# Kernel optimization log

Measured on AMD Instinct MI355X. Metric: run time of the kernel, lower is better.

The kernel has to match this reference:

```python
import jax, jax.numpy as jnp
import numpy as np

B, S, D, H = 2, 2048, 1024, 16
DK = D // H
WINDOW = 256


def _make_mask():
    # causal local-window sparsity: attend to j in (i-WINDOW, i]
    i = np.arange(S)[:, None]
    j = np.arange(S)[None, :]
    m = (j <= i) & (i - j < WINDOW)
    return jnp.asarray(m)


def setup_inputs() -> dict:
    key = jax.random.key(0)
    ks = jax.random.split(key, 9)
    sw = 1.0 / np.sqrt(D)
    return {
        "x": jax.random.normal(ks[0], (B, S, D), dtype=jnp.float32),
        "wq": jax.random.normal(ks[1], (D, D), dtype=jnp.float32) * sw,
        "bq": jnp.zeros((D,), dtype=jnp.float32),
        "wk": jax.random.normal(ks[2], (D, D), dtype=jnp.float32) * sw,
        "bk": jnp.zeros((D,), dtype=jnp.float32),
        "wv": jax.random.normal(ks[3], (D, D), dtype=jnp.float32) * sw,
        "bv": jnp.zeros((D,), dtype=jnp.float32),
        "wo": jax.random.normal(ks[4], (D, D), dtype=jnp.float32) * sw,
        "bo": jnp.zeros((D,), dtype=jnp.float32),
        "mask": _make_mask(),
    }


def reference(x, wq, bq, wk, bk, wv, bv, wo, bo, mask):
    b, s, d = x.shape
    # projections (torch Linear: x @ W.T + b), split heads -> [b, h, s, dk]
    def proj(w, bias):
        return (x @ w.T + bias).reshape(b, s, H, DK).transpose(0, 2, 1, 3)

    q = proj(wq, bq)
    k = proj(wk, bk)
    v = proj(wv, bv)

    scores = jnp.einsum("bhqd,bhkd->bhqk", q, k) / jnp.sqrt(jnp.float32(DK))
    scores = jnp.where(mask, scores, -jnp.inf)  # mask broadcasts over b, h
    attn = jax.nn.softmax(scores, axis=-1)
    out = jnp.einsum("bhqk,bhkd->bhqd", attn, v)
    out = out.transpose(0, 2, 1, 3).reshape(b, s, d)
    return out @ wo.T + bo
```

## Files before the change

kernel.cpp:

```cpp
#include <hip/hip_runtime.h>

#define S_LEN 2048
#define DMODEL 1024
#define NHEADS 16
#define WIN 256

typedef unsigned short u16;
typedef unsigned int u32;
typedef __attribute__((ext_vector_type(8))) __bf16 bf16x8;
typedef __attribute__((ext_vector_type(4))) float f32x4;
typedef __attribute__((ext_vector_type(8))) u16 u16x8;
typedef __attribute__((ext_vector_type(4))) u16 u16x4;

__device__ __forceinline__ u16 f2bf(float f) {
  u32 u = __builtin_bit_cast(u32, f);
  u += 0x7fffu + ((u >> 16) & 1u);
  return (u16)(u >> 16);
}

#define GLDS16(g, l) __builtin_amdgcn_global_load_lds( \
    (const __attribute__((address_space(1))) void*)(g), \
    (__attribute__((address_space(3))) void*)(l), 16, 0, 0)

__global__ __launch_bounds__(256) void cast_all(
    const float* __restrict__ x, const float* __restrict__ wq, const float* __restrict__ wk,
    const float* __restrict__ wv, const float* __restrict__ wo,
    u16* __restrict__ xb, u16* __restrict__ wqb, u16* __restrict__ wkb,
    u16* __restrict__ wvb, u16* __restrict__ wob) {
  const int e = (blockIdx.x * 256 + threadIdx.x) * 4;
  const float* src; u16* dst; int off;
  if (e < (1 << 22)) { src = x; dst = xb; off = e; }
  else {
    int r = e - (1 << 22);
    int seg = r >> 20; off = r & ((1 << 20) - 1);
    src = (seg == 0) ? wq : (seg == 1) ? wk : (seg == 2) ? wv : wo;
    dst = (seg == 0) ? wqb : (seg == 1) ? wkb : (seg == 2) ? wvb : wob;
  }
  float4 v = *(const float4*)(src + off);
  u16x4 o = { f2bf(v.x), f2bf(v.y), f2bf(v.z), f2bf(v.w) };
  *(u16x4*)(dst + off) = o;
}

__global__ __launch_bounds__(256) void gemm_nt(
    const u16* __restrict__ A,
    const u16* __restrict__ B0, const u16* __restrict__ B1, const u16* __restrict__ B2,
    const float* __restrict__ bias0, const float* __restrict__ bias1, const float* __restrict__ bias2,
    u16* __restrict__ C0, u16* __restrict__ C1, u16* __restrict__ C2,
    const int M, const int N, const int K)
{
  const u16* Bt; const float* bias; u16* C;
  if (blockIdx.z == 0)      { Bt = B0; bias = bias0; C = C0; }
  else if (blockIdx.z == 1) { Bt = B1; bias = bias1; C = C1; }
  else                      { Bt = B2; bias = bias2; C = C2; }

  __shared__ u16 As[2][128 * 32];
  __shared__ u16 Bs[2][128 * 32];

  const int t = threadIdx.x;
  const int row0 = blockIdx.x * 128;
  const int col0 = blockIdx.y * 128;
  const int lane = t & 63, lo = lane & 15, hi = lane >> 4;
  const int wv = t >> 6;
  const int wr = (wv >> 1) * 64, wc = (wv & 1) * 64;

  f32x4 acc[4][4];
  #pragma unroll
  for (int i = 0; i < 4; ++i)
    #pragma unroll
    for (int j = 0; j < 4; ++j) acc[i][j] = (f32x4)0.0f;

  const int NT = K >> 5;

  auto stage = [&](int buf, int kt) {
    const int kof = kt * 32;
    #pragma unroll
    for (int c = 0; c < 2; ++c) {
      const int off = t * 16 + c * 4096;
      const int r = off >> 6;
      const int ke = (off & 63) >> 1;
      GLDS16(A  + (size_t)(row0 + r) * K + (kof + ke), (u16*)As + buf * (128 * 32) + (off >> 1));
      GLDS16(Bt + (size_t)(col0 + r) * K + (kof + ke), (u16*)Bs + buf * (128 * 32) + (off >> 1));
    }
  };

  stage(0, 0);
  int cur = 0;
  for (int kt = 0; kt < NT; ++kt) {
    __syncthreads();
    if (kt + 1 < NT) stage(cur ^ 1, kt + 1);
    bf16x8 af[4], bfr[4];
    #pragma unroll
    for (int mi = 0; mi < 4; ++mi)
      af[mi] = *(const bf16x8*)&As[cur][(wr + mi * 16 + lo) * 32 + hi * 8];
    #pragma unroll
    for (int ni = 0; ni < 4; ++ni)
      bfr[ni] = *(const bf16x8*)&Bs[cur][(wc + ni * 16 + lo) * 32 + hi * 8];
    #pragma unroll
    for (int mi = 0; mi < 4; ++mi)
      #pragma unroll
      for (int ni = 0; ni < 4; ++ni)
        acc[mi][ni] = __builtin_amdgcn_mfma_f32_16x16x32_bf16(af[mi], bfr[ni], acc[mi][ni], 0, 0, 0);
    cur ^= 1;
  }

  #pragma unroll
  for (int mi = 0; mi < 4; ++mi) {
    #pragma unroll
    for (int ni = 0; ni < 4; ++ni) {
      const int col = col0 + wc + ni * 16 + lo;
      const float bv = bias[col];
      #pragma unroll
      for (int r = 0; r < 4; ++r) {
        const int row = row0 + wr + mi * 16 + hi * 4 + r;
        C[(size_t)row * N + col] = f2bf(acc[mi][ni][r] + bv);
      }
    }
  }
}

__global__ __launch_bounds__(256) void gemm_out64(
    const u16* __restrict__ A, const u16* __restrict__ Bt,
    const float* __restrict__ bias, float* __restrict__ C)
{
  constexpr int N = 1024, K = 1024;

  __shared__ u16 As[2][128 * 32];
  __shared__ u16 Bs[2][64 * 32];

  int id = blockIdx.y * gridDim.x + blockIdx.x;
  int wgid = (id & 7) * 64 + (id >> 3);
  const int row0 = (wgid >> 4) * 128;
  const int col0 = (wgid & 15) * 64;

  const int t = threadIdx.x;
  const int lane = t & 63, lo = lane & 15, hi = lane >> 4;
  const int wv = t >> 6;
  const int wr = (wv >> 1) * 64, wc = (wv & 1) * 32;

  f32x4 acc[4][2];
  #pragma unroll
  for (int i = 0; i < 4; ++i)
    #pragma unroll
    for (int j = 0; j < 2; ++j) acc[i][j] = (f32x4)0.0f;

  auto stage = [&](int buf, int kt) {
    const int kof = kt * 32;
    #pragma unroll
    for (int c = 0; c < 2; ++c) {
      const int off = t * 16 + c * 4096;
      const int r = off >> 6;
      const int ke = (off & 63) >> 1;
      GLDS16(A + (size_t)(row0 + r) * K + (kof + ke), (u16*)As + buf * (128 * 32) + (off >> 1));
    }
    {
      const int off = t * 16;
      const int r = off >> 6;
      const int ke = (off & 63) >> 1;
      GLDS16(Bt + (size_t)(col0 + r) * K + (kof + ke), (u16*)Bs + buf * (64 * 32) + (off >> 1));
    }
  };

  stage(0, 0);
  int cur = 0;
  for (int kt = 0; kt < (K >> 5); ++kt) {
    __syncthreads();
    if (kt + 1 < (K >> 5)) stage(cur ^ 1, kt + 1);
    bf16x8 af[4], bfr[2];
    #pragma unroll
    for (int mi = 0; mi < 4; ++mi)
      af[mi] = *(const bf16x8*)&As[cur][(wr + mi * 16 + lo) * 32 + hi * 8];
    #pragma unroll
    for (int ni = 0; ni < 2; ++ni)
      bfr[ni] = *(const bf16x8*)&Bs[cur][(wc + ni * 16 + lo) * 32 + hi * 8];
    #pragma unroll
    for (int mi = 0; mi < 4; ++mi)
      #pragma unroll
      for (int ni = 0; ni < 2; ++ni)
        acc[mi][ni] = __builtin_amdgcn_mfma_f32_16x16x32_bf16(af[mi], bfr[ni], acc[mi][ni], 0, 0, 0);
    cur ^= 1;
  }

  #pragma unroll
  for (int mi = 0; mi < 4; ++mi) {
    #pragma unroll
    for (int ni = 0; ni < 2; ++ni) {
      const int col = col0 + wc + ni * 16 + lo;
      const float bv = bias[col];
      #pragma unroll
      for (int r = 0; r < 4; ++r) {
        const int row = row0 + wr + mi * 16 + hi * 4 + r;
        C[(size_t)row * N + col] = acc[mi][ni][r] + bv;
      }
    }
  }
}

__device__ __forceinline__ int swzK(int row, int col) {
  int byte = (row << 7) + (col << 1);
  byte ^= (row & 7) << 4;
  return byte >> 1;
}
__device__ __forceinline__ int swzV(int d, int j) {
  int byte = (d << 7) + (j << 1);
  byte ^= ((d & 7) << 4) ^ (((d >> 4) & 3) << 5);
  return byte >> 1;
}

__global__ __launch_bounds__(256) void attn_win(const u16* __restrict__ Q,
                                                const u16* __restrict__ K,
                                                const u16* __restrict__ V,
                                                u16* __restrict__ O) {
  const int qt = blockIdx.x, h = blockIdx.y, b = blockIdx.z;
  const int q0 = qt * 64;
  const int t = threadIdx.x;
  const int wv = t >> 6, lane = t & 63, lo = lane & 15, hi = lane >> 4;

  __shared__ u16 Qs[64 * 64];
  __shared__ u16 Ks[2][64 * 64];
  __shared__ u16 Vt[2][64 * 64];
  __shared__ u16 Ps[4][16 * 64];

  const size_t base = ((size_t)b * S_LEN) * DMODEL + h * 64;

  #pragma unroll
  for (int c = 0; c < 2; ++c) {
    const int off = t * 16 + c * 4096;
    const int r = off >> 7, ce = (off & 127) >> 1;
    GLDS16(Q + base + (size_t)(q0 + r) * DMODEL + ce, (u16*)Qs + (off >> 1));
  }

  const int vrow = t >> 2;
  const int vc0  = (t & 3) * 16;
  const int ktmin = max(0, (256 - q0) >> 6);

  u16x8 kra, krb, vra, vrb;
  auto issue = [&](int kt) {
    const int jg = q0 - 256 + kt * 64 + vrow;
    if (jg >= 0) {
      const u16* sk = K + base + (size_t)jg * DMODEL + vc0;
      kra = *(const u16x8*)sk; krb = *(const u16x8*)(sk + 8);
      const u16* sv = V + base + (size_t)jg * DMODEL + vc0;
      vra = *(const u16x8*)sv; vrb = *(const u16x8*)(sv + 8);
    } else {
      kra = (u16x8)0; krb = (u16x8)0; vra = (u16x8)0; vrb = (u16x8)0;
    }
  };
  auto commit = [&](int buf) {
    *(u16x8*)&Ks[buf][swzK(vrow, vc0)]     = kra;
    *(u16x8*)&Ks[buf][swzK(vrow, vc0 + 8)] = krb;
    #pragma unroll
    for (int e = 0; e < 8; ++e) {
      Vt[buf][swzV(vc0 + e, vrow)]     = vra[e];
      Vt[buf][swzV(vc0 + 8 + e, vrow)] = vrb[e];
    }
  };

  issue(ktmin);
  commit(0);
  __syncthreads();

  bf16x8 qf[2];
  #pragma unroll
  for (int kq = 0; kq < 2; ++kq)
    qf[kq] = *(const bf16x8*)&Qs[(wv * 16 + lo) * 64 + kq * 32 + hi * 8];

  f32x4 oacc[4];
  #pragma unroll
  for (int i = 0; i < 4; ++i) oacc[i] = (f32x4)0.0f;
  float m_r[4] = {-1e30f, -1e30f, -1e30f, -1e30f};
  float l_r[4] = {0.f, 0.f, 0.f, 0.f};

  int cur = 0;
  for (int kt = ktmin; kt < 5; ++kt) {
    const int kstart = q0 - 256 + kt * 64;
    if (kt < 4) issue(kt + 1);

    f32x4 sfr[4];
    #pragma unroll
    for (int ni = 0; ni < 4; ++ni) {
      sfr[ni] = (f32x4)0.0f;
      #pragma unroll
      for (int kq = 0; kq < 2; ++kq) {
        bf16x8 kf = *(const bf16x8*)&Ks[cur][swzK(ni * 16 + lo, kq * 32 + hi * 8)];
        sfr[ni] = __builtin_amdgcn_mfma_f32_16x16x32_bf16(qf[kq], kf, sfr[ni], 0, 0, 0);
      }
    }

    float sv[4][4], cmax[4] = {-1e30f, -1e30f, -1e30f, -1e30f};
    const int i0 = q0 + wv * 16 + hi * 4;
    #pragma unroll
    for (int ni = 0; ni < 4; ++ni) {
      const int j = kstart + ni * 16 + lo;
      #pragma unroll
      for (int r = 0; r < 4; ++r) {
        const int i = i0 + r;
        float x = sfr[ni][r] * 0.125f;
        const bool ok = (j >= 0) & (j <= i) & (i - j < WIN);
        x = ok ? x : -1e30f;
        sv[ni][r] = x;
        cmax[r] = fmaxf(cmax[r], x);
      }
    }
    #pragma unroll
    for (int d = 1; d < 16; d <<= 1) {
      #pragma unroll
      for (int r = 0; r < 4; ++r) cmax[r] = fmaxf(cmax[r], __shfl_xor(cmax[r], d));
    }

    float pr[4][4], rsum[4];
    #pragma unroll
    for (int r = 0; r < 4; ++r) {
      const float mnew = fmaxf(m_r[r], cmax[r]);
      const float sc = __expf(m_r[r] - mnew);
      m_r[r] = mnew;
      l_r[r] *= sc;
      #pragma unroll
      for (int ni = 0; ni < 4; ++ni) oacc[ni][r] *= sc;
      float s = 0.f;
      #pragma unroll
      for (int ni = 0; ni < 4; ++ni) {
        const float p = __expf(sv[ni][r] - mnew);
        pr[ni][r] = p;
        s += p;
      }
      rsum[r] = s;
    }
    #pragma unroll
    for (int d = 1; d < 16; d <<= 1) {
      #pragma unroll
      for (int r = 0; r < 4; ++r) rsum[r] += __shfl_xor(rsum[r], d);
    }
    #pragma unroll
    for (int r = 0; r < 4; ++r) l_r[r] += rsum[r];

    #pragma unroll
    for (int ni = 0; ni < 4; ++ni)
      #pragma unroll
      for (int r = 0; r < 4; ++r)
        Ps[wv][swzK(hi * 4 + r, ni * 16 + lo)] = f2bf(pr[ni][r]);

    bf16x8 pa[2];
    #pragma unroll
    for (int kp = 0; kp < 2; ++kp)
      pa[kp] = *(const bf16x8*)&Ps[wv][swzK(lo, kp * 32 + hi * 8)];

    #pragma unroll
    for (int ni = 0; ni < 4; ++ni) {
      #pragma unroll
      for (int kp = 0; kp < 2; ++kp) {
        bf16x8 vf = *(const bf16x8*)&Vt[cur][swzV(ni * 16 + lo, kp * 32 + hi * 8)];
        oacc[ni] = __builtin_amdgcn_mfma_f32_16x16x32_bf16(pa[kp], vf, oacc[ni], 0, 0, 0);
      }
    }

    if (kt < 4) commit(cur ^ 1);
    __syncthreads();
    cur ^= 1;
  }

  #pragma unroll
  for (int ni = 0; ni < 4; ++ni) {
    #pragma unroll
    for (int r = 0; r < 4; ++r) {
      const int row = q0 + wv * 16 + hi * 4 + r;
      O[base + (size_t)row * DMODEL + ni * 16 + lo] = f2bf(oacc[ni][r] / l_r[r]);
    }
  }
}

extern "C" void kernel_launch(void* const* d_in, const int* in_sizes, int n_in,
                              void* d_out, int out_size, void* d_ws, size_t ws_size,
                              hipStream_t stream) {
  const float* x  = (const float*)d_in[0];
  const float* wq = (const float*)d_in[1];
  const float* bq = (const float*)d_in[2];
  const float* wk = (const float*)d_in[3];
  const float* bk = (const float*)d_in[4];
  const float* wvp = (const float*)d_in[5];
  const float* bv = (const float*)d_in[6];
  const float* wo = (const float*)d_in[7];
  const float* bo = (const float*)d_in[8];
  float* out = (float*)d_out;

  char* ws = (char*)d_ws;
  const size_t MB = 1024 * 1024;
  u16* xb  = (u16*)(ws);
  u16* wqb = (u16*)(ws + 8 * MB);
  u16* wkb = (u16*)(ws + 10 * MB);
  u16* wvb = (u16*)(ws + 12 * MB);
  u16* wob = (u16*)(ws + 14 * MB);
  u16* Qb  = (u16*)(ws + 16 * MB);
  u16* Kb  = (u16*)(ws + 24 * MB);
  u16* Vb  = (u16*)(ws + 32 * MB);
  u16* Ob  = (u16*)(ws + 40 * MB);

  cast_all<<<8192, 256, 0, stream>>>(x, wq, wk, wvp, wo, xb, wqb, wkb, wvb, wob);

  dim3 g1(4096 / 128, 1024 / 128, 3);
  gemm_nt<<<g1, 256, 0, stream>>>(xb, wqb, wkb, wvb, bq, bk, bv,
                                  Qb, Kb, Vb, 4096, 1024, 1024);

  attn_win<<<dim3(S_LEN / 64, NHEADS, 2), 256, 0, stream>>>(Qb, Kb, Vb, Ob);

  gemm_out64<<<dim3(32, 16), 256, 0, stream>>>(Ob, wob, bo, out);
}
```

Baseline: 94.71 us.

## Double attention query tile to 128 rows with 8 waves sharing K/V tiles

Result: no change. 95.28 us (+0.6%).

```diff
diff --git a/kernel.cpp b/kernel.cpp
--- a/kernel.cpp
+++ b/kernel.cpp
@@ -206,64 +206,61 @@
   return byte >> 1;
 }
 
-__global__ __launch_bounds__(256) void attn_win(const u16* __restrict__ Q,
+__global__ __launch_bounds__(512) void attn_win(const u16* __restrict__ Q,
                                                 const u16* __restrict__ K,
                                                 const u16* __restrict__ V,
                                                 u16* __restrict__ O) {
   const int qt = blockIdx.x, h = blockIdx.y, b = blockIdx.z;
-  const int q0 = qt * 64;
+  const int q0 = qt * 128;
   const int t = threadIdx.x;
   const int wv = t >> 6, lane = t & 63, lo = lane & 15, hi = lane >> 4;
 
-  __shared__ u16 Qs[64 * 64];
   __shared__ u16 Ks[2][64 * 64];
   __shared__ u16 Vt[2][64 * 64];
-  __shared__ u16 Ps[4][16 * 64];
+  __shared__ u16 Ps[8][16 * 64];
 
   const size_t base = ((size_t)b * S_LEN) * DMODEL + h * 64;
-
-  #pragma unroll
-  for (int c = 0; c < 2; ++c) {
-    const int off = t * 16 + c * 4096;
-    const int r = off >> 7, ce = (off & 127) >> 1;
-    GLDS16(Q + base + (size_t)(q0 + r) * DMODEL + ce, (u16*)Qs + (off >> 1));
-  }
-
-  const int vrow = t >> 2;
-  const int vc0  = (t & 3) * 16;
+  const int w0 = q0 + wv * 16;
+
+  bf16x8 qf[2];
+  {
+    const u16* qp = Q + base + (size_t)(w0 + lo) * DMODEL;
+    u16x8 qa = *(const u16x8*)(qp + hi * 8);
+    u16x8 qb = *(const u16x8*)(qp + 32 + hi * 8);
+    union { u16x8 s; bf16x8 v; } ua, ub;
+    #pragma unroll
+    for (int e = 0; e < 8; ++e) {
+      float fa = __builtin_bit_cast(float, (u32)qa[e] << 16) * 0.125f;
+      float fb = __builtin_bit_cast(float, (u32)qb[e] << 16) * 0.125f;
+      ua.s[e] = (u16)(__builtin_bit_cast(u32, fa) >> 16);
+      ub.s[e] = (u16)(__builtin_bit_cast(u32, fb) >> 16);
+    }
+    qf[0] = ua.v; qf[1] = ub.v;
+  }
+
+  const int vrow = t >> 3;
+  const int vc0  = (t & 7) * 8;
   const int ktmin = max(0, (256 - q0) >> 6);
 
-  u16x8 kra, krb, vra, vrb;
+  u16x8 kra, vra;
   auto issue = [&](int kt) {
     const int jg = q0 - 256 + kt * 64 + vrow;
     if (jg >= 0) {
-      const u16* sk = K + base + (size_t)jg * DMODEL + vc0;
-      kra = *(const u16x8*)sk; krb = *(const u16x8*)(sk + 8);
-      const u16* sv = V + base + (size_t)jg * DMODEL + vc0;
-      vra = *(const u16x8*)sv; vrb = *(const u16x8*)(sv + 8);
-    } else {
-      kra = (u16x8)0; krb = (u16x8)0; vra = (u16x8)0; vrb = (u16x8)0;
-    }
+      kra = *(const u16x8*)(K + base + (size_t)jg * DMODEL + vc0);
+      vra = *(const u16x8*)(V + base + (size_t)jg * DMODEL + vc0);
+    } else { kra = (u16x8)0; vra = (u16x8)0; }
   };
   auto commit = [&](int buf) {
-    *(u16x8*)&Ks[buf][swzK(vrow, vc0)]     = kra;
-    *(u16x8*)&Ks[buf][swzK(vrow, vc0 + 8)] = krb;
-    #pragma unroll
-    for (int e = 0; e < 8; ++e) {
-      Vt[buf][swzV(vc0 + e, vrow)]     = vra[e];
-      Vt[buf][swzV(vc0 + 8 + e, vrow)] = vrb[e];
-    }
+    *(u16x8*)&Ks[buf][swzK(vrow, vc0)] = kra;
+    #pragma unroll
+    for (int e = 0; e < 8; ++e)
+      Vt[buf][swzV(vc0 + e, vrow)] = vra[e];
   };
 
   issue(ktmin);
   commit(0);
   __syncthreads();
 
-  bf16x8 qf[2];
-  #pragma unroll
-  for (int kq = 0; kq < 2; ++kq)
-    qf[kq] = *(const bf16x8*)&Qs[(wv * 16 + lo) * 64 + kq * 32 + hi * 8];
-
   f32x4 oacc[4];
   #pragma unroll
   for (int i = 0; i < 4; ++i) oacc[i] = (f32x4)0.0f;
@@ -271,89 +268,92 @@
   float l_r[4] = {0.f, 0.f, 0.f, 0.f};
 
   int cur = 0;
-  for (int kt = ktmin; kt < 5; ++kt) {
+  for (int kt = ktmin; kt < 6; ++kt) {
     const int kstart = q0 - 256 + kt * 64;
-    if (kt < 4) issue(kt + 1);
-
-    f32x4 sfr[4];
-    #pragma unroll
-    for (int ni = 0; ni < 4; ++ni) {
-      sfr[ni] = (f32x4)0.0f;
-      #pragma unroll
-      for (int kq = 0; kq < 2; ++kq) {
-        bf16x8 kf = *(const bf16x8*)&Ks[cur][swzK(ni * 16 + lo, kq * 32 + hi * 8)];
-        sfr[ni] = __builtin_amdgcn_mfma_f32_16x16x32_bf16(qf[kq], kf, sfr[ni], 0, 0, 0);
-      }
-    }
-
-    float sv[4][4], cmax[4] = {-1e30f, -1e30f, -1e30f, -1e30f};
-    const int i0 = q0 + wv * 16 + hi * 4;
-    #pragma unroll
-    for (int ni = 0; ni < 4; ++ni) {
-      const int j = kstart + ni * 16 + lo;
+    if (kt < 5) issue(kt + 1);
+
+    const bool act = (kstart <= w0 + 15) && (kstart + 63 >= w0 - 255);
+    if (act) {
+      f32x4 sfr[4];
+      #pragma unroll
+      for (int ni = 0; ni < 4; ++ni) {
+        sfr[ni] = (f32x4)0.0f;
+        #pragma unroll
+        for (int kq = 0; kq < 2; ++kq) {
+          bf16x8 kf = *(const bf16x8*)&Ks[cur][swzK(ni * 16 + lo, kq * 32 + hi * 8)];
+          sfr[ni] = __builtin_amdgcn_mfma_f32_16x16x32_bf16(qf[kq], kf, sfr[ni], 0, 0, 0);
+        }
+      }
+
+      float sv[4][4], cmax[4] = {-1e30f, -1e30f, -1e30f, -1e30f};
+      const int i0 = w0 + hi * 4;
+      #pragma unroll
+      for (int ni = 0; ni < 4; ++ni) {
+        const int j = kstart + ni * 16 + lo;
+        #pragma unroll
+        for (int r = 0; r < 4; ++r) {
+          const int i = i0 + r;
+          float x = sfr[ni][r];
+          const bool ok = (j >= 0) & (j <= i) & (i - j < WIN);
+          x = ok ? x : -1e30f;
+          sv[ni][r] = x;
+          cmax[r] = fmaxf(cmax[r], x);
+        }
+      }
+      #pragma unroll
+      for (int d = 1; d < 16; d <<= 1) {
+        #pragma unroll
+        for (int r = 0; r < 4; ++r) cmax[r] = fmaxf(cmax[r], __shfl_xor(cmax[r], d));
+      }
+
+      float pr[4][4], rsum[4];
       #pragma unroll
       for (int r = 0; r < 4; ++r) {
-        const int i = i0 + r;
-        float x = sfr[ni][r] * 0.125f;
-        const bool ok = (j >= 0) & (j <= i) & (i - j < WIN);
-        x = ok ? x : -1e30f;
-        sv[ni][r] = x;
-        cmax[r] = fmaxf(cmax[r], x);
-      }
-    }
-    #pragma unroll
-    for (int d = 1; d < 16; d <<= 1) {
-      #pragma unroll
-      for (int r = 0; r < 4; ++r) cmax[r] = fmaxf(cmax[r], __shfl_xor(cmax[r], d));
-    }
-
-    float pr[4][4], rsum[4];
-    #pragma unroll
-    for (int r = 0; r < 4; ++r) {
-      const float mnew = fmaxf(m_r[r], cmax[r]);
-      const float sc = __expf(m_r[r] - mnew);
-      m_r[r] = mnew;
-      l_r[r] *= sc;
-      #pragma unroll
-      for (int ni = 0; ni < 4; ++ni) oacc[ni][r] *= sc;
-      float s = 0.f;
+        const float mnew = fmaxf(m_r[r], cmax[r]);
+        const float sc = __expf(m_r[r] - mnew);
+        m_r[r] = mnew;
+        l_r[r] *= sc;
+        #pragma unroll
+        for (int ni = 0; ni < 4; ++ni) oacc[ni][r] *= sc;
+        float s = 0.f;
+        #pragma unroll
+        for (int ni = 0; ni < 4; ++ni) {
+          const float p = __expf(sv[ni][r] - mnew);
+          pr[ni][r] = p;
+          s += p;
+        }
+        rsum[r] = s;
+      }
+      #pragma unroll
+      for (int d = 1; d < 16; d <<= 1) {
+        #pragma unroll
+        for (int r = 0; r < 4; ++r) rsum[r] += __shfl_xor(rsum[r], d);
+      }
+      #pragma unroll
+      for (int r = 0; r < 4; ++r) l_r[r] += rsum[r];
+
+      #pragma unroll
+      for (int ni = 0; ni < 4; ++ni)
+        #pragma unroll
+        for (int r = 0; r < 4; ++r)
+          Ps[wv][swzK(hi * 4 + r, ni * 16 + lo)] = f2bf(pr[ni][r]);
+
+      bf16x8 pa[2];
+      #pragma unroll
+      for (int kp = 0; kp < 2; ++kp)
+        pa[kp] = *(const bf16x8*)&Ps[wv][swzK(lo, kp * 32 + hi * 8)];
+
       #pragma unroll
       for (int ni = 0; ni < 4; ++ni) {
-        const float p = __expf(sv[ni][r] - mnew);
-        pr[ni][r] = p;
-        s += p;
-      }
-      rsum[r] = s;
-    }
-    #pragma unroll
-    for (int d = 1; d < 16; d <<= 1) {
-      #pragma unroll
-      for (int r = 0; r < 4; ++r) rsum[r] += __shfl_xor(rsum[r], d);
-    }
-    #pragma unroll
-    for (int r = 0; r < 4; ++r) l_r[r] += rsum[r];
-
-    #pragma unroll
-    for (int ni = 0; ni < 4; ++ni)
-      #pragma unroll
-      for (int r = 0; r < 4; ++r)
-        Ps[wv][swzK(hi * 4 + r, ni * 16 + lo)] = f2bf(pr[ni][r]);
-
-    bf16x8 pa[2];
-    #pragma unroll
-    for (int kp = 0; kp < 2; ++kp)
-      pa[kp] = *(const bf16x8*)&Ps[wv][swzK(lo, kp * 32 + hi * 8)];
-
-    #pragma unroll
-    for (int ni = 0; ni < 4; ++ni) {
-      #pragma unroll
-      for (int kp = 0; kp < 2; ++kp) {
-        bf16x8 vf = *(const bf16x8*)&Vt[cur][swzV(ni * 16 + lo, kp * 32 + hi * 8)];
-        oacc[ni] = __builtin_amdgcn_mfma_f32_16x16x32_bf16(pa[kp], vf, oacc[ni], 0, 0, 0);
-      }
-    }
-
-    if (kt < 4) commit(cur ^ 1);
+        #pragma unroll
+        for (int kp = 0; kp < 2; ++kp) {
+          bf16x8 vf = *(const bf16x8*)&Vt[cur][swzV(ni * 16 + lo, kp * 32 + hi * 8)];
+          oacc[ni] = __builtin_amdgcn_mfma_f32_16x16x32_bf16(pa[kp], vf, oacc[ni], 0, 0, 0);
+        }
+      }
+    }
+
+    if (kt < 5) commit(cur ^ 1);
     __syncthreads();
     cur ^= 1;
   }
@@ -362,7 +362,7 @@
   for (int ni = 0; ni < 4; ++ni) {
     #pragma unroll
     for (int r = 0; r < 4; ++r) {
-      const int row = q0 + wv * 16 + hi * 4 + r;
+      const int row = w0 + hi * 4 + r;
       O[base + (size_t)row * DMODEL + ni * 16 + lo] = f2bf(oacc[ni][r] / l_r[r]);
     }
   }
@@ -400,7 +400,7 @@
   gemm_nt<<<g1, 256, 0, stream>>>(xb, wqb, wkb, wvb, bq, bk, bv,
                                   Qb, Kb, Vb, 4096, 1024, 1024);
 
-  attn_win<<<dim3(S_LEN / 64, NHEADS, 2), 256, 0, stream>>>(Qb, Kb, Vb, Ob);
+  attn_win<<<dim3(S_LEN / 128, NHEADS, 2), 512, 0, stream>>>(Qb, Kb, Vb, Ob);
 
   gemm_out64<<<dim3(32, 16), 256, 0, stream>>>(Ob, wob, bo, out);
 }
```
